# Kernel optimization log

Hardware: AMD Instinct MI355X
Metric: run time of the kernel (lower is better)

## Reference

```python
import jax, jax.numpy as jnp
import numpy as np

R_CUT = 5.0
N_NODES = 50000
N_EDGES = 400000
N_GRAPHS = 2500
D = 128        # embedding_size (hardcoded by torch.split(..., 128))
N_RBF = 20
N_BLOCKS = 3
PI = 3.141592653589793


def setup_inputs() -> dict:
    key = jax.random.key(0)
    ks = jax.random.split(key, 32)
    w = lambda k, s: (jax.random.normal(k, s) * 0.05).astype(jnp.float32)
    z = jax.random.randint(ks[0], (N_NODES,), 0, 100)
    edges = jax.random.randint(ks[1], (N_EDGES, 2), 0, N_NODES)
    r_ij = jax.random.uniform(ks[2], (N_EDGES, 1), minval=0.8, maxval=R_CUT, dtype=jnp.float32)
    d = jax.random.normal(ks[3], (N_EDGES, 3), dtype=jnp.float32)
    r_ij_normalized = d / jnp.linalg.norm(d, axis=1, keepdims=True)
    graph_idx = jax.random.randint(ks[4], (N_NODES,), 0, N_GRAPHS)
    return {
        "z": z, "edges": edges, "r_ij": r_ij,
        "r_ij_normalized": r_ij_normalized, "graph_idx": graph_idx,
        "emb": w(ks[5], (100, D)),
        # message blocks (stacked over N_BLOCKS)
        "msg_w1": w(ks[6], (N_BLOCKS, D, D)),   "msg_b1": w(ks[7], (N_BLOCKS, D)),
        "msg_w2": w(ks[8], (N_BLOCKS, D, 3 * D)), "msg_b2": w(ks[9], (N_BLOCKS, 3 * D)),
        "rbf_w": w(ks[10], (N_BLOCKS, N_RBF, 3 * D)), "rbf_b": w(ks[11], (N_BLOCKS, 3 * D)),
        # update blocks
        "upd_U": w(ks[12], (N_BLOCKS, D, D)), "upd_V": w(ks[13], (N_BLOCKS, D, D)),
        "upd_w1": w(ks[14], (N_BLOCKS, 2 * D, D)), "upd_b1": w(ks[15], (N_BLOCKS, D)),
        "upd_w2": w(ks[16], (N_BLOCKS, D, 3 * D)), "upd_b2": w(ks[17], (N_BLOCKS, 3 * D)),
        # readout
        "blue_w1": w(ks[18], (D, D)), "blue_b1": w(ks[19], (D,)),
        "blue_w2": w(ks[20], (D, 1)), "blue_b2": w(ks[21], (1,)),
    }


def _rbf(r, r_cut):
    n = jnp.arange(1, N_RBF + 1, dtype=r.dtype)  # [20]
    return jnp.sin(n * PI / r_cut * r) / r        # [E,20]


def _fcut(r, r_cut):
    return jnp.where(r <= r_cut, 0.5 * (jnp.cos(PI * r / r_cut) + 1.0), 0.0)


def painn_forward(z, edges, r_ij, r_ij_normalized, graph_idx, emb,
                  msg_w1, msg_b1, msg_w2, msg_b2, rbf_w, rbf_b,
                  upd_U, upd_V, upd_w1, upd_b1, upd_w2, upd_b2,
                  blue_w1, blue_b1, blue_w2, blue_b2):
    silu = jax.nn.silu
    src = edges[:, 1]  # gathered (neighbor j)
    dst = edges[:, 0]  # scattered (center i)
    s = emb[z]                                           # [N,128]
    v = jnp.zeros((s.shape[0], 3, D), dtype=r_ij.dtype)  # [N,3,128]
    rbf = _rbf(r_ij, R_CUT)                              # [E,20]
    f_c = _fcut(r_ij, R_CUT)                             # [E,1]
    for i in range(N_BLOCKS):
        # --- message block ---
        rbf_fcut = (rbf @ rbf_w[i] + rbf_b[i]) * f_c            # [E,384]
        s_pass = silu(s @ msg_w1[i] + msg_b1[i]) @ msg_w2[i] + msg_b2[i]  # [N,384]
        pass_out = rbf_fcut * s_pass[src]                        # [E,384]
        d_v, d_s, d_rep = jnp.split(pass_out, 3, axis=-1)        # each [E,128]
        delta_v = v[src] * d_v[:, None, :] + r_ij_normalized[:, :, None] * d_rep[:, None, :]
        s = s + jax.ops.segment_sum(d_s, dst, num_segments=N_NODES)
        v = v + jax.ops.segment_sum(delta_v, dst, num_segments=N_NODES)
        # --- update block ---
        U_v = jnp.einsum('nde,ef->ndf', v, upd_U[i])             # [N,3,128]
        V_v = jnp.einsum('nde,ef->ndf', v, upd_V[i])
        V_norm = jnp.linalg.norm(V_v, axis=1)                    # [N,128]
        sv = jnp.concatenate([V_norm, s], axis=1)                # [N,256]
        a = silu(sv @ upd_w1[i] + upd_b1[i]) @ upd_w2[i] + upd_b2[i]  # [N,384]
        avv, asv, ass = jnp.split(a, 3, axis=1)
        s = s + jnp.sum(U_v * V_v, axis=1) * asv + ass
        v = v + avv[:, None, :] * U_v
    blue = silu(s @ blue_w1 + blue_b1) @ blue_w2 + blue_b2       # [N,1]
    return jax.ops.segment_sum(blue, graph_idx, num_segments=N_GRAPHS)  # [G,1]


def reference(z, edges, r_ij, r_ij_normalized, graph_idx, emb,
              msg_w1, msg_b1, msg_w2, msg_b2, rbf_w, rbf_b,
              upd_U, upd_V, upd_w1, upd_b1, upd_w2, upd_b2,
              blue_w1, blue_b1, blue_w2, blue_b2):
    return painn_forward(z, edges, r_ij, r_ij_normalized, graph_idx, emb,
                         msg_w1, msg_b1, msg_w2, msg_b2, rbf_w, rbf_b,
                         upd_U, upd_V, upd_w1, upd_b1, upd_w2, upd_b2,
                         blue_w1, blue_b1, blue_w2, blue_b2)
```

## Files before the change

kernel.cpp:

```cpp
#include <hip/hip_runtime.h>
#include <hip/hip_bf16.h>
#include <math.h>

#define N_NODES 50000
#define N_EDGES 400000
#define N_GRAPHS 2500
#define D 128
#define D3 384
#define N_RBF 20
#define R_CUT 5.0f
#define PI_F 3.14159265358979f
#define NCH 98
#define EPT_STRIDE 24

typedef __attribute__((ext_vector_type(8))) short bf16x8;
typedef __attribute__((ext_vector_type(4))) float f32x4;

__device__ __forceinline__ float silu_f(float x) {
    return x / (1.0f + __expf(-x));
}
__device__ __forceinline__ short f2bf(float x) {
    union { float f; unsigned u; } v; v.f = x;
    unsigned r = (v.u + 0x7FFFu + ((v.u >> 16) & 1u)) >> 16;
    return (short)r;
}
__device__ __forceinline__ float bf2f(short x) {
    union { unsigned u; float f; } v; v.u = ((unsigned)(unsigned short)x) << 16;
    return v.f;
}

#define MAXJOBS 19
struct PackJobs {
    const float* W[MAXJOBS];
    short* P[MAXJOBS];
    int K[MAXJOBS];
    int N[MAXJOBS];
    int boff[MAXJOBS + 1];
    int njobs;
};
__global__ void k_packall(PackJobs jobs) {
    int b = blockIdx.x;
    int j = 0;
    while (j + 1 < jobs.njobs && b >= jobs.boff[j + 1]) ++j;
    int t = (b - jobs.boff[j]) * 256 + threadIdx.x;
    int K = jobs.K[j], N = jobs.N[j];
    int NKT = K / 32;
    int total = (N / 16) * NKT * 64;
    if (t >= total) return;
    const float* W = jobs.W[j];
    short* P = jobs.P[j];
    int lane = t & 63;
    int kt = (t >> 6) % NKT;
    int nt = (t >> 6) / NKT;
    int k0 = kt * 32 + (lane >> 4) * 8;
    int col = nt * 16 + (lane & 15);
    #pragma unroll
    for (int q = 0; q < 8; ++q)
        P[(size_t)t * 8 + q] = f2bf(W[(size_t)(k0 + q) * N + col]);
}

template<int K, int N, bool SILU, int AMODE>
__global__ __launch_bounds__(256) void k_gemm(const void* __restrict__ Aptr,
                                              const void* __restrict__ A2ptr,
                                              const short* __restrict__ Bp,
                                              const float* __restrict__ bias,
                                              short* __restrict__ Cbf, int M) {
    constexpr int NKT = K / 32, NNT = N / 16;
    int lane = threadIdx.x & 63, wv = threadIdx.x >> 6;
    int tile = blockIdx.x * 4 + wv;
    if (tile * 16 >= M) return;
    int arow = tile * 16 + (lane & 15);
    int kgrp = (lane >> 4) * 8;

    bf16x8 a[NKT];
    if (AMODE == 0) {
        const short* A = (const short*)Aptr + (size_t)arow * K + kgrp;
        #pragma unroll
        for (int kt = 0; kt < NKT; ++kt) a[kt] = *(const bf16x8*)(A + kt * 32);
    } else if (AMODE == 1) {
        const float* A = (const float*)Aptr + (size_t)arow * K + kgrp;
        #pragma unroll
        for (int kt = 0; kt < NKT; ++kt)
            #pragma unroll
            for (int j = 0; j < 8; ++j) a[kt][j] = f2bf(A[kt * 32 + j]);
    } else {
        const short* A1 = (const short*)Aptr + (size_t)arow * 128 + kgrp;
        const float* A2 = (const float*)A2ptr + (size_t)arow * 128 + kgrp;
        #pragma unroll
        for (int kt = 0; kt < 4 && kt < NKT; ++kt) a[kt] = *(const bf16x8*)(A1 + kt * 32);
        #pragma unroll
        for (int kt = 4; kt < NKT; ++kt)
            #pragma unroll
            for (int j = 0; j < 8; ++j) a[kt][j] = f2bf(A2[(kt - 4) * 32 + j]);
    }

    int crow0 = tile * 16 + (lane >> 4) * 4;
    int ccol = lane & 15;
    const bf16x8* Bv = (const bf16x8*)Bp;
    #pragma unroll
    for (int nt = 0; nt < NNT; ++nt) {
        f32x4 acc = {0.f, 0.f, 0.f, 0.f};
        #pragma unroll
        for (int kt = 0; kt < NKT; ++kt) {
            bf16x8 b = Bv[(nt * NKT + kt) * 64 + lane];
            acc = __builtin_amdgcn_mfma_f32_16x16x32_bf16(a[kt], b, acc, 0, 0, 0);
        }
        int col = nt * 16 + ccol;
        float bs = bias ? bias[col] : 0.0f;
        #pragma unroll
        for (int j = 0; j < 4; ++j) {
            float v = acc[j] + bs;
            if (SILU) v = silu_f(v);
            Cbf[(size_t)(crow0 + j) * N + col] = f2bf(v);
        }
    }
}

__global__ void k_embed(const int* __restrict__ z, const float* __restrict__ emb,
                        float* __restrict__ s) {
    int i = blockIdx.x * blockDim.x + threadIdx.x;
    if (i < N_NODES * D) {
        int n = i >> 7, c = i & 127;
        s[i] = emb[z[n] * D + c];
    }
}

__global__ void k_hist(const int* __restrict__ edges, int* __restrict__ cnt) {
    int e = blockIdx.x * 256 + threadIdx.x;
    if (e < N_EDGES) atomicAdd(&cnt[edges[2 * e]], 1);
}

__global__ void k_scan1(const int* __restrict__ cnt, int* __restrict__ csum) {
    int t = threadIdx.x;
    int g = blockIdx.x * 512 + t;
    int v = (g < N_NODES) ? cnt[g] : 0;
    #pragma unroll
    for (int off = 32; off > 0; off >>= 1) v += __shfl_down(v, off, 64);
    __shared__ int ws[8];
    if ((t & 63) == 0) ws[t >> 6] = v;
    __syncthreads();
    if (t == 0) {
        int sum = 0;
        #pragma unroll
        for (int i = 0; i < 8; ++i) sum += ws[i];
        csum[blockIdx.x] = sum;
    }
}

__global__ void k_scan2(const int* __restrict__ csum, int* __restrict__ cbase) {
    if (threadIdx.x == 0 && blockIdx.x == 0) {
        int s = 0;
        for (int i = 0; i < NCH; ++i) { cbase[i] = s; s += csum[i]; }
    }
}

__global__ void k_scan3(const int* __restrict__ cnt, const int* __restrict__ cbase,
                        int* __restrict__ rowptr) {
    __shared__ int buf[512];
    int t = threadIdx.x;
    int g = blockIdx.x * 512 + t;
    int orig = (g < N_NODES) ? cnt[g] : 0;
    buf[t] = orig;
    __syncthreads();
    for (int off = 1; off < 512; off <<= 1) {
        int v = (t >= off) ? buf[t - off] : 0;
        __syncthreads();
        buf[t] += v;
        __syncthreads();
    }
    if (g < N_NODES) rowptr[g] = cbase[blockIdx.x] + buf[t] - orig;
    if (g == 0 && blockIdx.x == 0) rowptr[N_NODES] = N_EDGES;
}

__global__ void k_scatter(const int* __restrict__ edges, const float* __restrict__ r_ij,
                          const float* __restrict__ rhat, const int* __restrict__ rowptr,
                          int* __restrict__ cursor, int* __restrict__ esrc,
                          float* __restrict__ ept) {
    int e = blockIdx.x * 256 + threadIdx.x;
    if (e >= N_EDGES) return;
    int dst = edges[2 * e], src = edges[2 * e + 1];
    int p = rowptr[dst] + atomicAdd(&cursor[dst], 1);
    esrc[p] = src;
    float r = r_ij[e];
    float fc = (r <= R_CUT) ? 0.5f * (cosf(PI_F * r / R_CUT) + 1.0f) : 0.0f;
    float inv_r = 1.0f / r;
    float* rec = ept + (size_t)p * EPT_STRIDE;
    #pragma unroll
    for (int k = 0; k < N_RBF; ++k) {
        float rb = sinf((float)(k + 1) * (PI_F / R_CUT) * r) * inv_r;
        rec[k] = rb * fc;
    }
    rec[20] = fc;
    rec[21] = rhat[3 * e];
    rec[22] = rhat[3 * e + 1];
    rec[23] = rhat[3 * e + 2];
}

__global__ __launch_bounds__(128, 4) void k_edge2(
    const int* __restrict__ rowptr, const int* __restrict__ esrc,
    const float* __restrict__ ept,
    const float* __restrict__ rbf_w, const float* __restrict__ rbf_b,
    const short* __restrict__ spass, const short* __restrict__ vold,
    float* __restrict__ s, short* __restrict__ vnew) {
    int c = threadIdx.x;
    float w0[N_RBF], w1[N_RBF], w2[N_RBF];
    #pragma unroll
    for (int k = 0; k < N_RBF; ++k) {
        w0[k] = rbf_w[k * D3 + c];
        w1[k] = rbf_w[k * D3 + 128 + c];
        w2[k] = rbf_w[k * D3 + 256 + c];
    }
    float b0 = rbf_b[c], b1 = rbf_b[128 + c], b2 = rbf_b[256 + c];
    for (int n = blockIdx.x; n < N_NODES; n += gridDim.x) {
        int p0 = rowptr[n], p1 = rowptr[n + 1];
        float sa = 0.f, va0 = 0.f, va1 = 0.f, va2 = 0.f;
        for (int p = p0; p < p1; ++p) {
            const float4* e4 = (const float4*)(ept + (size_t)p * EPT_STRIDE);
            float4 q0 = e4[0], q1 = e4[1], q2 = e4[2], q3 = e4[3], q4 = e4[4], q5 = e4[5];
            int src = esrc[p];
            float a0, a1, a2;
            float fc = q5.x;
            a0 = b0 * fc; a1 = b1 * fc; a2 = b2 * fc;
            float rv[20] = {q0.x, q0.y, q0.z, q0.w, q1.x, q1.y, q1.z, q1.w,
                            q2.x, q2.y, q2.z, q2.w, q3.x, q3.y, q3.z, q3.w,
                            q4.x, q4.y, q4.z, q4.w};
            #pragma unroll
            for (int k = 0; k < N_RBF; ++k) {
                a0 += rv[k] * w0[k];
                a1 += rv[k] * w1[k];
                a2 += rv[k] * w2[k];
            }
            const short* sp = spass + (size_t)src * D3;
            float dv = a0 * bf2f(sp[c]);
            float ds = a1 * bf2f(sp[128 + c]);
            float dr = a2 * bf2f(sp[256 + c]);
            sa += ds;
            const short* vs = vold + (size_t)src * D3;
            va0 += bf2f(vs[c]) * dv + q5.y * dr;
            va1 += bf2f(vs[128 + c]) * dv + q5.z * dr;
            va2 += bf2f(vs[256 + c]) * dv + q5.w * dr;
        }
        s[(size_t)n * D + c] += sa;
        size_t vb = (size_t)n * D3;
        vnew[vb + c]       = f2bf(bf2f(vold[vb + c]) + va0);
        vnew[vb + 128 + c] = f2bf(bf2f(vold[vb + 128 + c]) + va1);
        vnew[vb + 256 + c] = f2bf(bf2f(vold[vb + 256 + c]) + va2);
    }
}

__global__ void k_svbuild(const short* __restrict__ Vv, short* __restrict__ Vn) {
    int i = blockIdx.x * 256 + threadIdx.x;
    int n = i >> 7, c = i & 127;
    float acc = 0.f;
    #pragma unroll
    for (int d = 0; d < 3; ++d) {
        float v = bf2f(Vv[(size_t)(n * 3 + d) * D + c]);
        acc += v * v;
    }
    Vn[i] = f2bf(sqrtf(acc));
}

__global__ void k_apply(float* __restrict__ s, short* __restrict__ v,
                        const short* __restrict__ Uv, const short* __restrict__ Vv,
                        const short* __restrict__ a_bf) {
    int i = blockIdx.x * 256 + threadIdx.x;
    int n = i >> 7, c = i & 127;
    float avv = bf2f(a_bf[(size_t)n * D3 + c]);
    float asv = bf2f(a_bf[(size_t)n * D3 + 128 + c]);
    float ass = bf2f(a_bf[(size_t)n * D3 + 256 + c]);
    float scal = 0.f;
    float uvr[3];
    #pragma unroll
    for (int d = 0; d < 3; ++d) {
        float u = bf2f(Uv[(size_t)(n * 3 + d) * D + c]);
        float vv = bf2f(Vv[(size_t)(n * 3 + d) * D + c]);
        uvr[d] = u;
        scal += u * vv;
    }
    s[i] += scal * asv + ass;
    #pragma unroll
    for (int d = 0; d < 3; ++d) {
        size_t idx = (size_t)n * D3 + d * 128 + c;
        v[idx] = f2bf(bf2f(v[idx]) + avv * uvr[d]);
    }
}

__global__ void k_blue_dot(const short* __restrict__ h, const int* __restrict__ graph_idx,
                           const float* __restrict__ w2, const float* __restrict__ b2,
                           float* __restrict__ out) {
    __shared__ float red[4];
    int c = threadIdx.x & 127;
    int n = blockIdx.x * 2 + (threadIdx.x >> 7);
    float val = bf2f(h[(size_t)n * D + c]) * w2[c];
    #pragma unroll
    for (int off = 32; off > 0; off >>= 1) val += __shfl_down(val, off, 64);
    if ((threadIdx.x & 63) == 0) red[threadIdx.x >> 6] = val;
    __syncthreads();
    if (threadIdx.x == 0)   atomicAdd(&out[graph_idx[n]], red[0] + red[1] + b2[0]);
    if (threadIdx.x == 128) atomicAdd(&out[graph_idx[n]], red[2] + red[3] + b2[0]);
}

static inline int gemm_grid(int M) { return (M / 16 + 3) / 4; }

extern "C" void kernel_launch(void* const* d_in, const int* in_sizes, int n_in,
                              void* d_out, int out_size, void* d_ws, size_t ws_size,
                              hipStream_t stream) {
    const int*   z         = (const int*)d_in[0];
    const int*   edges     = (const int*)d_in[1];
    const float* r_ij      = (const float*)d_in[2];
    const float* rhat      = (const float*)d_in[3];
    const int*   graph_idx = (const int*)d_in[4];
    const float* emb       = (const float*)d_in[5];
    const float* msg_w1    = (const float*)d_in[6];
    const float* msg_b1    = (const float*)d_in[7];
    const float* msg_w2    = (const float*)d_in[8];
    const float* msg_b2    = (const float*)d_in[9];
    const float* rbf_w     = (const float*)d_in[10];
    const float* rbf_b     = (const float*)d_in[11];
    const float* upd_U     = (const float*)d_in[12];
    const float* upd_V     = (const float*)d_in[13];
    const float* upd_w1    = (const float*)d_in[14];
    const float* upd_b1    = (const float*)d_in[15];
    const float* upd_w2    = (const float*)d_in[16];
    const float* upd_b2    = (const float*)d_in[17];
    const float* blue_w1   = (const float*)d_in[18];
    const float* blue_b1   = (const float*)d_in[19];
    const float* blue_w2   = (const float*)d_in[20];
    const float* blue_b2   = (const float*)d_in[21];
    float* out = (float*)d_out;

    char* ws = (char*)d_ws;
    size_t off = 0;
    auto alloc = [&](size_t bytes) { void* p = ws + off; off += (bytes + 255) & ~(size_t)255; return p; };

    float* s      = (float*)alloc((size_t)N_NODES * D * 4);
    short* bufV0  = (short*)alloc((size_t)N_NODES * D3 * 2);
    short* bufV1  = (short*)alloc((size_t)N_NODES * D3 * 2);
    short* shrd   = (short*)alloc((size_t)N_NODES * D3 * 2);
    short* hbuf   = (short*)alloc((size_t)N_NODES * D * 2);
    short* Vv     = (short*)alloc((size_t)N_NODES * D3 * 2);
    short* Vn     = shrd;
    int*    esrc   = (int*)alloc((size_t)N_EDGES * 4);
    float*  ept    = (float*)alloc((size_t)N_EDGES * EPT_STRIDE * 4);
    int*    rowptr = (int*)alloc((size_t)(N_NODES + 1) * 4);
    int*    cnt    = (int*)alloc((size_t)N_NODES * 4);
    int*    csum   = (int*)alloc(NCH * 4);
    int*    cbase  = (int*)alloc(NCH * 4);

    short* pBlue = (short*)alloc(16384 * 2);
    short* pMsgW1[3]; short* pMsgW2[3]; short* pU[3]; short* pV[3]; short* pUpdW1[3]; short* pUpdW2[3];
    for (int i = 0; i < 3; ++i) {
        pMsgW1[i] = (short*)alloc(16384 * 2);
        pMsgW2[i] = (short*)alloc(49152 * 2);
        pU[i]     = (short*)alloc(16384 * 2);
        pV[i]     = (short*)alloc(16384 * 2);
        pUpdW1[i] = (short*)alloc(32768 * 2);
        pUpdW2[i] = (short*)alloc(49152 * 2);
    }

    PackJobs jobs;
    jobs.njobs = 0;
    int bacc = 0;
    auto addjob = [&](const float* W, short* P, int K, int N) {
        int j = jobs.njobs++;
        jobs.W[j] = W; jobs.P[j] = P; jobs.K[j] = K; jobs.N[j] = N;
        jobs.boff[j] = bacc;
        int total = (N / 16) * (K / 32) * 64;
        bacc += (total + 255) / 256;
        jobs.boff[j + 1] = bacc;
    };
    addjob(blue_w1, pBlue, 128, 128);
    for (int i = 0; i < 3; ++i) {
        addjob(msg_w1 + (size_t)i * D * D,     pMsgW1[i], 128, 128);
        addjob(msg_w2 + (size_t)i * D * D3,    pMsgW2[i], 128, 384);
        addjob(upd_U  + (size_t)i * D * D,     pU[i],     128, 128);
        addjob(upd_V  + (size_t)i * D * D,     pV[i],     128, 128);
        addjob(upd_w1 + (size_t)i * 2 * D * D, pUpdW1[i], 256, 128);
        addjob(upd_w2 + (size_t)i * D * D3,    pUpdW2[i], 128, 384);
    }
    k_packall<<<bacc, 256, 0, stream>>>(jobs);

    hipMemsetAsync(cnt, 0, (size_t)N_NODES * 4, stream);
    k_hist<<<(N_EDGES + 255) / 256, 256, 0, stream>>>(edges, cnt);
    k_scan1<<<NCH, 512, 0, stream>>>(cnt, csum);
    k_scan2<<<1, 64, 0, stream>>>(csum, cbase);
    k_scan3<<<NCH, 512, 0, stream>>>(cnt, cbase, rowptr);
    hipMemsetAsync(cnt, 0, (size_t)N_NODES * 4, stream);
    k_scatter<<<(N_EDGES + 255) / 256, 256, 0, stream>>>(edges, r_ij, rhat, rowptr, cnt,
                                                         esrc, ept);

    hipMemsetAsync(bufV0, 0, (size_t)N_NODES * D3 * 2, stream);
    hipMemsetAsync(d_out, 0, (size_t)out_size * sizeof(float), stream);
    k_embed<<<(N_NODES * D) / 256, 256, 0, stream>>>(z, emb, s);

    const int gN  = gemm_grid(N_NODES);
    const int gN3 = gemm_grid(N_NODES * 3);

    for (int i = 0; i < 3; ++i) {
        short* vstate = (i & 1) ? bufV1 : bufV0;
        short* vscr   = (i & 1) ? bufV0 : bufV1;
        k_gemm<128, 128, true, 1><<<gN, 256, 0, stream>>>(
            s, nullptr, pMsgW1[i], msg_b1 + (size_t)i * D, hbuf, N_NODES);
        k_gemm<128, 384, false, 0><<<gN, 256, 0, stream>>>(
            hbuf, nullptr, pMsgW2[i], msg_b2 + (size_t)i * D3, shrd, N_NODES);
        k_edge2<<<4096, 128, 0, stream>>>(rowptr, esrc, ept,
                                          rbf_w + (size_t)i * N_RBF * D3,
                                          rbf_b + (size_t)i * D3,
                                          shrd, vstate, s, vscr);
        k_gemm<128, 128, false, 0><<<gN3, 256, 0, stream>>>(
            vscr, nullptr, pU[i], nullptr, vstate, N_NODES * 3);
        k_gemm<128, 128, false, 0><<<gN3, 256, 0, stream>>>(
            vscr, nullptr, pV[i], nullptr, Vv, N_NODES * 3);
        k_svbuild<<<(N_NODES * D) / 256, 256, 0, stream>>>(Vv, Vn);
        k_gemm<256, 128, true, 2><<<gN, 256, 0, stream>>>(
            Vn, s, pUpdW1[i], upd_b1 + (size_t)i * D, hbuf, N_NODES);
        k_gemm<128, 384, false, 0><<<gN, 256, 0, stream>>>(
            hbuf, nullptr, pUpdW2[i], upd_b2 + (size_t)i * D3, shrd, N_NODES);
        k_apply<<<(N_NODES * D) / 256, 256, 0, stream>>>(s, vscr, vstate, Vv, shrd);
    }

    k_gemm<128, 128, true, 1><<<gN, 256, 0, stream>>>(
        s, nullptr, pBlue, blue_b1, hbuf, N_NODES);
    k_blue_dot<<<N_NODES / 2, 256, 0, stream>>>(hbuf, graph_idx, blue_w2, blue_b2, out);
}
```

Before: 1.174 ms.

## Compute edge RBF filter with MFMA per 16-edge batch via LDS

The per-edge RBF-to-filter projection (20x384 FMAs per edge per channel) moves from scalar FMAs with weights held in registers to a bf16 MFMA 16x16x32 over batches of 16 edges. The gates go through shared memory before the per-edge message accumulation. Edge features are now stored as packed bf16 (32 shorts including fcut as the bias column) plus a separate float4 for the unit vector, which shrinks per-edge memory traffic. The trade-off is lower precision on the RBF values and gates, extra __syncthreads per batch, wasted MFMA work when a node has fewer than 16 edges, and a halved grid size.

After: 1.131 ms. 3.7% less time.

```diff
diff --git a/kernel.cpp b/kernel.cpp
--- a/kernel.cpp
+++ b/kernel.cpp
@@ -11,7 +11,7 @@
 #define R_CUT 5.0f
 #define PI_F 3.14159265358979f
 #define NCH 98
-#define EPT_STRIDE 24
+#define GEB 16
 
 typedef __attribute__((ext_vector_type(8))) short bf16x8;
 typedef __attribute__((ext_vector_type(4))) float f32x4;
@@ -59,6 +59,27 @@
         P[(size_t)t * 8 + q] = f2bf(W[(size_t)(k0 + q) * N + col]);
 }
 
+__global__ void k_packrbf(const float* __restrict__ rbf_w, const float* __restrict__ rbf_b,
+                          short* __restrict__ P) {
+    int t = blockIdx.x * 256 + threadIdx.x;
+    if (t >= 3 * 1536) return;
+    int i = t / 1536;
+    int r = t - i * 1536;
+    int lane = r & 63;
+    int nt = r >> 6;
+    int col = nt * 16 + (lane & 15);
+    int k0 = (lane >> 4) * 8;
+    const float* W = rbf_w + (size_t)i * N_RBF * D3;
+    const float* B = rbf_b + (size_t)i * D3;
+    short* out = P + (size_t)i * 12288 + (size_t)r * 8;
+    #pragma unroll
+    for (int q = 0; q < 8; ++q) {
+        int k = k0 + q;
+        float v = (k < N_RBF) ? W[(size_t)k * D3 + col] : ((k == N_RBF) ? B[col] : 0.0f);
+        out[q] = f2bf(v);
+    }
+}
+
 template<int K, int N, bool SILU, int AMODE>
 __global__ __launch_bounds__(256) void k_gemm(const void* __restrict__ Aptr,
                                               const void* __restrict__ A2ptr,
@@ -175,7 +196,7 @@
 __global__ void k_scatter(const int* __restrict__ edges, const float* __restrict__ r_ij,
                           const float* __restrict__ rhat, const int* __restrict__ rowptr,
                           int* __restrict__ cursor, int* __restrict__ esrc,
-                          float* __restrict__ ept) {
+                          short* __restrict__ erbf, float4* __restrict__ erhat) {
     int e = blockIdx.x * 256 + threadIdx.x;
     if (e >= N_EDGES) return;
     int dst = edges[2 * e], src = edges[2 * e + 1];
@@ -184,61 +205,73 @@
     float r = r_ij[e];
     float fc = (r <= R_CUT) ? 0.5f * (cosf(PI_F * r / R_CUT) + 1.0f) : 0.0f;
     float inv_r = 1.0f / r;
-    float* rec = ept + (size_t)p * EPT_STRIDE;
-    #pragma unroll
-    for (int k = 0; k < N_RBF; ++k) {
-        float rb = sinf((float)(k + 1) * (PI_F / R_CUT) * r) * inv_r;
-        rec[k] = rb * fc;
-    }
-    rec[20] = fc;
-    rec[21] = rhat[3 * e];
-    rec[22] = rhat[3 * e + 1];
-    rec[23] = rhat[3 * e + 2];
-}
-
-__global__ __launch_bounds__(128, 4) void k_edge2(
+    short rec[32];
+    #pragma unroll
+    for (int k = 0; k < N_RBF; ++k)
+        rec[k] = f2bf(sinf((float)(k + 1) * (PI_F / R_CUT) * r) * inv_r * fc);
+    rec[20] = f2bf(fc);
+    #pragma unroll
+    for (int k = 21; k < 32; ++k) rec[k] = 0;
+    short* out = erbf + (size_t)p * 32;
+    #pragma unroll
+    for (int k = 0; k < 32; ++k) out[k] = rec[k];
+    float4 rh;
+    rh.x = rhat[3 * e]; rh.y = rhat[3 * e + 1]; rh.z = rhat[3 * e + 2]; rh.w = 0.f;
+    erhat[p] = rh;
+}
+
+__global__ __launch_bounds__(128, 4) void k_edge3(
     const int* __restrict__ rowptr, const int* __restrict__ esrc,
-    const float* __restrict__ ept,
-    const float* __restrict__ rbf_w, const float* __restrict__ rbf_b,
+    const short* __restrict__ erbf, const float4* __restrict__ erhat,
+    const short* __restrict__ pRbf,
     const short* __restrict__ spass, const short* __restrict__ vold,
     float* __restrict__ s, short* __restrict__ vnew) {
-    int c = threadIdx.x;
-    float w0[N_RBF], w1[N_RBF], w2[N_RBF];
-    #pragma unroll
-    for (int k = 0; k < N_RBF; ++k) {
-        w0[k] = rbf_w[k * D3 + c];
-        w1[k] = rbf_w[k * D3 + 128 + c];
-        w2[k] = rbf_w[k * D3 + 256 + c];
-    }
-    float b0 = rbf_b[c], b1 = rbf_b[128 + c], b2 = rbf_b[256 + c];
+    __shared__ short gate_lds[GEB][D3];
+    int tid = threadIdx.x;
+    int lane = tid & 63;
+    int wv = tid >> 6;
+    int c = tid;
+    int ntb = wv * 12;
     for (int n = blockIdx.x; n < N_NODES; n += gridDim.x) {
         int p0 = rowptr[n], p1 = rowptr[n + 1];
         float sa = 0.f, va0 = 0.f, va1 = 0.f, va2 = 0.f;
-        for (int p = p0; p < p1; ++p) {
-            const float4* e4 = (const float4*)(ept + (size_t)p * EPT_STRIDE);
-            float4 q0 = e4[0], q1 = e4[1], q2 = e4[2], q3 = e4[3], q4 = e4[4], q5 = e4[5];
-            int src = esrc[p];
-            float a0, a1, a2;
-            float fc = q5.x;
-            a0 = b0 * fc; a1 = b1 * fc; a2 = b2 * fc;
-            float rv[20] = {q0.x, q0.y, q0.z, q0.w, q1.x, q1.y, q1.z, q1.w,
-                            q2.x, q2.y, q2.z, q2.w, q3.x, q3.y, q3.z, q3.w,
-                            q4.x, q4.y, q4.z, q4.w};
+        for (int pb = p0; pb < p1; pb += GEB) {
+            int erow = pb + (lane & 15);
+            if (erow >= p1) erow = p1 - 1;
+            bf16x8 afrag = *(const bf16x8*)(erbf + (size_t)erow * 32 + (lane >> 4) * 8);
+            int r0 = (lane >> 4) * 4;
+            int fcol = lane & 15;
             #pragma unroll
-            for (int k = 0; k < N_RBF; ++k) {
-                a0 += rv[k] * w0[k];
-                a1 += rv[k] * w1[k];
-                a2 += rv[k] * w2[k];
+            for (int t = 0; t < 12; ++t) {
+                int nt = ntb + t;
+                bf16x8 b = *(const bf16x8*)(pRbf + ((size_t)(nt * 64 + lane)) * 8);
+                f32x4 acc = {0.f, 0.f, 0.f, 0.f};
+                acc = __builtin_amdgcn_mfma_f32_16x16x32_bf16(afrag, b, acc, 0, 0, 0);
+                int col = nt * 16 + fcol;
+                #pragma unroll
+                for (int j = 0; j < 4; ++j)
+                    gate_lds[r0 + j][col] = f2bf(acc[j]);
             }
-            const short* sp = spass + (size_t)src * D3;
-            float dv = a0 * bf2f(sp[c]);
-            float ds = a1 * bf2f(sp[128 + c]);
-            float dr = a2 * bf2f(sp[256 + c]);
-            sa += ds;
-            const short* vs = vold + (size_t)src * D3;
-            va0 += bf2f(vs[c]) * dv + q5.y * dr;
-            va1 += bf2f(vs[128 + c]) * dv + q5.z * dr;
-            va2 += bf2f(vs[256 + c]) * dv + q5.w * dr;
+            __syncthreads();
+            int pe = (pb + GEB < p1) ? pb + GEB : p1;
+            for (int p = pb; p < pe; ++p) {
+                int src = esrc[p];
+                float4 rh = erhat[p];
+                const short* g = gate_lds[p - pb];
+                float a0 = bf2f(g[c]);
+                float a1 = bf2f(g[128 + c]);
+                float a2 = bf2f(g[256 + c]);
+                const short* sp = spass + (size_t)src * D3;
+                float dv = a0 * bf2f(sp[c]);
+                float ds = a1 * bf2f(sp[128 + c]);
+                float dr = a2 * bf2f(sp[256 + c]);
+                sa += ds;
+                const short* vs = vold + (size_t)src * D3;
+                va0 += bf2f(vs[c]) * dv + rh.x * dr;
+                va1 += bf2f(vs[128 + c]) * dv + rh.y * dr;
+                va2 += bf2f(vs[256 + c]) * dv + rh.z * dr;
+            }
+            __syncthreads();
         }
         s[(size_t)n * D + c] += sa;
         size_t vb = (size_t)n * D3;
@@ -341,13 +374,15 @@
     short* Vv     = (short*)alloc((size_t)N_NODES * D3 * 2);
     short* Vn     = shrd;
     int*    esrc   = (int*)alloc((size_t)N_EDGES * 4);
-    float*  ept    = (float*)alloc((size_t)N_EDGES * EPT_STRIDE * 4);
+    short*  erbf   = (short*)alloc((size_t)N_EDGES * 32 * 2);
+    float4* erhat  = (float4*)alloc((size_t)N_EDGES * 16);
     int*    rowptr = (int*)alloc((size_t)(N_NODES + 1) * 4);
     int*    cnt    = (int*)alloc((size_t)N_NODES * 4);
     int*    csum   = (int*)alloc(NCH * 4);
     int*    cbase  = (int*)alloc(NCH * 4);
 
     short* pBlue = (short*)alloc(16384 * 2);
+    short* pRbfAll = (short*)alloc((size_t)3 * 12288 * 2);
     short* pMsgW1[3]; short* pMsgW2[3]; short* pU[3]; short* pV[3]; short* pUpdW1[3]; short* pUpdW2[3];
     for (int i = 0; i < 3; ++i) {
         pMsgW1[i] = (short*)alloc(16384 * 2);
@@ -379,6 +414,7 @@
         addjob(upd_w2 + (size_t)i * D * D3,    pUpdW2[i], 128, 384);
     }
     k_packall<<<bacc, 256, 0, stream>>>(jobs);
+    k_packrbf<<<18, 256, 0, stream>>>(rbf_w, rbf_b, pRbfAll);
 
     hipMemsetAsync(cnt, 0, (size_t)N_NODES * 4, stream);
     k_hist<<<(N_EDGES + 255) / 256, 256, 0, stream>>>(edges, cnt);
@@ -387,7 +423,7 @@
     k_scan3<<<NCH, 512, 0, stream>>>(cnt, cbase, rowptr);
     hipMemsetAsync(cnt, 0, (size_t)N_NODES * 4, stream);
     k_scatter<<<(N_EDGES + 255) / 256, 256, 0, stream>>>(edges, r_ij, rhat, rowptr, cnt,
-                                                         esrc, ept);
+                                                         esrc, erbf, erhat);
 
     hipMemsetAsync(bufV0, 0, (size_t)N_NODES * D3 * 2, stream);
     hipMemsetAsync(d_out, 0, (size_t)out_size * sizeof(float), stream);
@@ -403,9 +439,8 @@
             s, nullptr, pMsgW1[i], msg_b1 + (size_t)i * D, hbuf, N_NODES);
         k_gemm<128, 384, false, 0><<<gN, 256, 0, stream>>>(
             hbuf, nullptr, pMsgW2[i], msg_b2 + (size_t)i * D3, shrd, N_NODES);
-        k_edge2<<<4096, 128, 0, stream>>>(rowptr, esrc, ept,
-                                          rbf_w + (size_t)i * N_RBF * D3,
-                                          rbf_b + (size_t)i * D3,
+        k_edge3<<<2048, 128, 0, stream>>>(rowptr, esrc, erbf, erhat,
+                                          pRbfAll + (size_t)i * 12288,
                                           shrd, vstate, s, vscr);
         k_gemm<128, 128, false, 0><<<gN3, 256, 0, stream>>>(
             vscr, nullptr, pU[i], nullptr, vstate, N_NODES * 3);
```
